# Optimization experiments

Hardware: AMD Instinct MI355X
Metric: run time of the kernel (lower is better)

## Reference

```python
import jax, jax.numpy as jnp
import numpy as np

N_HEAD = 16
N_KV_HEAD = 4
HEAD_DIM = 128
RMS_EPS = 1.1920928955078125e-07  # torch float32 eps used by F.rms_norm default


def apply_rotary_emb(x, cos, sin):
    # x: [B,T,H,D]; cos/sin: [1,T,1,D/2]
    d = x.shape[-1] // 2
    x1, x2 = x[..., :d], x[..., d:]
    return jnp.concatenate([x1 * cos + x2 * sin, -x1 * sin + x2 * cos], axis=-1)


def rms_norm(x):
    return x * jax.lax.rsqrt(jnp.mean(x * x, axis=-1, keepdims=True) + RMS_EPS)


def setup_inputs() -> dict:
    key = jax.random.key(0)
    ks = jax.random.split(key, 7)
    B, T, C = 2, 2048, 2048
    return {
        "x": jax.random.normal(ks[0], (B, T, C), jnp.float32),
        "cos": jax.random.normal(ks[1], (1, T, 1, HEAD_DIM // 2), jnp.float32),
        "sin": jax.random.normal(ks[2], (1, T, 1, HEAD_DIM // 2), jnp.float32),
        "wq": jax.random.normal(ks[3], (C, N_HEAD * HEAD_DIM), jnp.float32) * 0.02,
        "wk": jax.random.normal(ks[4], (C, N_KV_HEAD * HEAD_DIM), jnp.float32) * 0.02,
        "wv": jax.random.normal(ks[5], (C, N_KV_HEAD * HEAD_DIM), jnp.float32) * 0.02,
        "wo": jax.random.normal(ks[6], (C, C), jnp.float32) * 0.02,
        "window_size": 512,
    }


def reference(x, cos, sin, wq, wk, wv, wo, window_size):
    B, T, C = x.shape
    H, KV, D = N_HEAD, N_KV_HEAD, HEAD_DIM
    rep = H // KV
    q = (x @ wq).reshape(B, T, H, D)
    k = (x @ wk).reshape(B, T, KV, D)
    v = (x @ wv).reshape(B, T, KV, D)
    q = rms_norm(apply_rotary_emb(q, cos, sin))
    k = rms_norm(apply_rotary_emb(k, cos, sin))
    # GQA: group query heads by kv head instead of materializing expanded K/V
    qg = q.reshape(B, T, KV, rep, D)
    scale = 1.0 / np.sqrt(D)
    scores = jnp.einsum('btkrd,bskd->bkrts', qg, k) * scale  # [B,KV,rep,T,S]
    row = jnp.arange(T)[:, None]
    col = jnp.arange(T)[None, :]
    mask = (col <= row) & (row - col <= window_size)  # causal & sliding window
    scores = jnp.where(mask, scores, jnp.finfo(scores.dtype).min)
    probs = jax.nn.softmax(scores, axis=-1)
    y = jnp.einsum('bkrts,bskd->btkrd', probs, v).reshape(B, T, H * D)
    return y @ wo
```

## Files before the change

### kernel.cpp

```cpp
#include <hip/hip_runtime.h>
#include <stdint.h>

typedef __attribute__((ext_vector_type(4))) float f32x4;
typedef __attribute__((ext_vector_type(8))) __bf16 bf16x8;
typedef __attribute__((ext_vector_type(4))) unsigned int u32x4;
typedef unsigned short u16;

#define B_DIM 2
#define T_DIM 2048
#define C_DIM 2048
#define H_Q   16
#define H_KV  4
#define HD    128
#define NQKV  3072
#define MTOK  4096
#define RMS_EPS 1.1920928955078125e-07f

__device__ __forceinline__ u16 f2bf(float f) {
  union { float f; unsigned int u; } v; v.f = f;
  unsigned int r = v.u + 0x7FFFu + ((v.u >> 16) & 1u);
  return (u16)(r >> 16);
}
__device__ __forceinline__ float bf2f(u16 h) {
  union { unsigned int u; float f; } v; v.u = ((unsigned int)h) << 16;
  return v.f;
}
__device__ __forceinline__ f32x4 mfma16(bf16x8 a, bf16x8 b, f32x4 c) {
  return __builtin_amdgcn_mfma_f32_16x16x32_bf16(a, b, c, 0, 0, 0);
}

__global__ __launch_bounds__(256) void cast_x_kernel(const float* __restrict__ x,
                                                     u16* __restrict__ xb, int n) {
  int i = (blockIdx.x * 256 + threadIdx.x) * 4;
  if (i >= n) return;
  float4 v = *(const float4*)(x + i);
  u16 o0 = f2bf(v.x), o1 = f2bf(v.y), o2 = f2bf(v.z), o3 = f2bf(v.w);
  unsigned int lo = (unsigned int)o0 | ((unsigned int)o1 << 16);
  unsigned int hi = (unsigned int)o2 | ((unsigned int)o3 << 16);
  *(uint2*)(xb + i) = make_uint2(lo, hi);
}

__global__ __launch_bounds__(256) void transpose_cast_kernel(const float* __restrict__ in,
                                                             u16* __restrict__ out,
                                                             int K, int N) {
  __shared__ float tile[64][65];
  int n0 = blockIdx.x * 64, k0 = blockIdx.y * 64;
  int t = threadIdx.x;
  #pragma unroll
  for (int idx = t; idx < 4096; idx += 256) {
    int r = idx >> 6, c = idx & 63;
    tile[r][c] = in[(size_t)(k0 + r) * N + n0 + c];
  }
  __syncthreads();
  #pragma unroll
  for (int idx = t; idx < 4096; idx += 256) {
    int r = idx >> 6, c = idx & 63;
    out[(size_t)(n0 + r) * K + k0 + c] = f2bf(tile[c][r]);
  }
}

__global__ __launch_bounds__(256) void rope_rms_kernel(u16* __restrict__ qkv,
                                                       const float* __restrict__ cosb,
                                                       const float* __restrict__ sinb) {
  int gw = (blockIdx.x * 256 + threadIdx.x) >> 6;
  int lane = threadIdx.x & 63;
  int hh = gw % (H_Q + H_KV);
  int tok = gw / (H_Q + H_KV);
  int t = tok & (T_DIM - 1);
  int base = (hh < H_Q) ? hh * HD : (C_DIM + (hh - H_Q) * HD);
  u16* p = qkv + (size_t)tok * NQKV + base;
  float x1 = bf2f(p[lane]);
  float x2 = bf2f(p[lane + 64]);
  float c = cosb[t * 64 + lane];
  float s = sinb[t * 64 + lane];
  float o1 =  x1 * c + x2 * s;
  float o2 = -x1 * s + x2 * c;
  float ss = o1 * o1 + o2 * o2;
  #pragma unroll
  for (int off = 1; off < 64; off <<= 1) ss += __shfl_xor(ss, off);
  float r = rsqrtf(ss * (1.0f / 128.0f) + RMS_EPS);
  p[lane]      = f2bf(o1 * r);
  p[lane + 64] = f2bf(o2 * r);
}

template<int BF16OUT>
__global__ __launch_bounds__(256) void gemm_bt_kernel(const u16* __restrict__ A,
                                                      const u16* __restrict__ Bt,
                                                      void* __restrict__ Cv,
                                                      int M, int N, int K) {
  __shared__ __align__(16) u16 Asm[128 * 64];
  __shared__ __align__(16) u16 Bsm[128 * 64];
  const int tid = threadIdx.x;
  const int lane = tid & 63;
  const int wid = tid >> 6;
  const int m0 = blockIdx.y * 128, n0 = blockIdx.x * 128;
  const int wm = (wid >> 1) * 64, wn = (wid & 1) * 64;
  const int l15 = lane & 15, l4 = lane >> 4;
  f32x4 acc[4][4] = {};

  for (int k0 = 0; k0 < K; k0 += 64) {
    __syncthreads();
    #pragma unroll
    for (int i = 0; i < 4; ++i) {
      int cid = tid + i * 256;
      int row = cid >> 3, c = cid & 7;
      int dst = row * 128 + ((c ^ (row & 7)) * 16);
      u32x4 va = *(const u32x4*)(A  + (size_t)(m0 + row) * K + k0 + c * 8);
      *(u32x4*)((char*)Asm + dst) = va;
      u32x4 vb = *(const u32x4*)(Bt + (size_t)(n0 + row) * K + k0 + c * 8);
      *(u32x4*)((char*)Bsm + dst) = vb;
    }
    __syncthreads();
    #pragma unroll
    for (int ks = 0; ks < 2; ++ks) {
      bf16x8 af[4], bfr[4];
      #pragma unroll
      for (int mf = 0; mf < 4; ++mf) {
        int r = wm + mf * 16 + l15;
        int bo = r * 128 + (((ks * 4 + l4) ^ (r & 7)) * 16);
        af[mf] = __builtin_bit_cast(bf16x8, *(const u32x4*)((const char*)Asm + bo));
      }
      #pragma unroll
      for (int nf = 0; nf < 4; ++nf) {
        int r = wn + nf * 16 + l15;
        int bo = r * 128 + (((ks * 4 + l4) ^ (r & 7)) * 16);
        bfr[nf] = __builtin_bit_cast(bf16x8, *(const u32x4*)((const char*)Bsm + bo));
      }
      #pragma unroll
      for (int mf = 0; mf < 4; ++mf)
        #pragma unroll
        for (int nf = 0; nf < 4; ++nf)
          acc[mf][nf] = mfma16(af[mf], bfr[nf], acc[mf][nf]);
    }
  }
  #pragma unroll
  for (int mf = 0; mf < 4; ++mf)
    #pragma unroll
    for (int nf = 0; nf < 4; ++nf)
      #pragma unroll
      for (int reg = 0; reg < 4; ++reg) {
        int row = m0 + wm + mf * 16 + l4 * 4 + reg;
        int col = n0 + wn + nf * 16 + l15;
        float v = acc[mf][nf][reg];
        if (BF16OUT) ((u16*)Cv)[(size_t)row * N + col] = f2bf(v);
        else         ((float*)Cv)[(size_t)row * N + col] = v;
      }
}

__global__ __launch_bounds__(256) void attn_kernel(const u16* __restrict__ qkv,
                                                   u16* __restrict__ yb,
                                                   const int* __restrict__ wsz_p) {
  __shared__ __align__(16) u16 Ksm[64 * 128];
  __shared__ __align__(16) u16 Vsm[128 * 64];
  __shared__ __align__(16) u16 Psm[4 * 16 * 64];

  const int W = wsz_p[0];
  const int tid = threadIdx.x, lane = tid & 63, wid = tid >> 6;
  const int l15 = lane & 15, l4 = lane >> 4;
  const int bid = blockIdx.x;
  const int qt  = bid & 31;
  const int h   = (bid >> 5) & 15;
  const int b   = bid >> 9;
  const int kvh = h >> 2;
  const size_t tokb = (size_t)b * T_DIM;

  bf16x8 qf[4];
  {
    int r = qt * 64 + wid * 16 + l15;
    const u16* qp = qkv + (tokb + r) * NQKV + h * HD;
    #pragma unroll
    for (int ks = 0; ks < 4; ++ks)
      qf[ks] = __builtin_bit_cast(bf16x8, *(const u32x4*)(qp + ks * 32 + l4 * 8));
  }

  f32x4 yacc[8] = {};
  float mrow[4], lrow[4];
  #pragma unroll
  for (int rg = 0; rg < 4; ++rg) { mrow[rg] = -3.0e38f; lrow[rg] = 0.0f; }

  const float sc = 0.08838834764831845f * 1.4426950408889634f;
  const int rbase = qt * 64 + wid * 16;
  int smin = qt * 64 - W; if (smin < 0) smin = 0;
  const int t0 = smin >> 6;

  for (int kt = t0; kt <= qt; ++kt) {
    __syncthreads();
    {
      const u16* kp = qkv + (tokb + kt * 64) * NQKV + C_DIM + kvh * HD;
      #pragma unroll
      for (int i = 0; i < 4; ++i) {
        int cid = tid + i * 256;
        int key = cid >> 4, c = cid & 15;
        u32x4 v = *(const u32x4*)(kp + (size_t)key * NQKV + c * 8);
        *(u32x4*)((char*)Ksm + key * 256 + ((c ^ (key & 7)) * 16)) = v;
      }
    }
    {
      const u16* vp = qkv + (tokb + kt * 64) * NQKV + C_DIM + H_KV * HD + kvh * HD;
      int d = tid & 127, g = tid >> 7;
      #pragma unroll
      for (int cc = 0; cc < 4; ++cc) {
        int kc = g * 4 + cc;
        u16 vals[8];
        #pragma unroll
        for (int j = 0; j < 8; ++j)
          vals[j] = vp[(size_t)(kc * 8 + j) * NQKV + d];
        u32x4 w;
        w.x = (unsigned int)vals[0] | ((unsigned int)vals[1] << 16);
        w.y = (unsigned int)vals[2] | ((unsigned int)vals[3] << 16);
        w.z = (unsigned int)vals[4] | ((unsigned int)vals[5] << 16);
        w.w = (unsigned int)vals[6] | ((unsigned int)vals[7] << 16);
        *(u32x4*)((char*)Vsm + d * 128 + ((kc ^ (d & 7)) * 16)) = w;
      }
    }
    __syncthreads();

    float Sc[4][4];
    #pragma unroll
    for (int nf = 0; nf < 4; ++nf) {
      f32x4 sa = {0.f, 0.f, 0.f, 0.f};
      int key = nf * 16 + l15;
      #pragma unroll
      for (int ks = 0; ks < 4; ++ks) {
        int bo = key * 256 + (((ks * 4 + l4) ^ (key & 7)) * 16);
        bf16x8 kf = __builtin_bit_cast(bf16x8, *(const u32x4*)((const char*)Ksm + bo));
        sa = mfma16(qf[ks], kf, sa);
      }
      #pragma unroll
      for (int rg = 0; rg < 4; ++rg) Sc[nf][rg] = sa[rg] * sc;
    }

    const int slo = kt * 64;
    bool fullvalid = ((slo + 63) <= rbase) && ((rbase + 15 - slo) <= W);
    if (!fullvalid) {
      #pragma unroll
      for (int nf = 0; nf < 4; ++nf) {
        int s = slo + nf * 16 + l15;
        #pragma unroll
        for (int rg = 0; rg < 4; ++rg) {
          int r = rbase + l4 * 4 + rg;
          if (s > r || (r - s) > W) Sc[nf][rg] = -3.0e38f;
        }
      }
    }

    float f[4];
    #pragma unroll
    for (int rg = 0; rg < 4; ++rg) {
      float tm = fmaxf(fmaxf(Sc[0][rg], Sc[1][rg]), fmaxf(Sc[2][rg], Sc[3][rg]));
      #pragma unroll
      for (int off = 1; off < 16; off <<= 1) tm = fmaxf(tm, __shfl_xor(tm, off));
      float mnew = fmaxf(mrow[rg], tm);
      float mo = fmaxf(mrow[rg], -1.0e30f);
      float mc = fmaxf(mnew,     -1.0e30f);
      f[rg] = exp2f(mo - mc);
      mrow[rg] = mnew;
    }
    float rs[4] = {0.f, 0.f, 0.f, 0.f};
    u16 pb[4][4];
    #pragma unroll
    for (int nf = 0; nf < 4; ++nf)
      #pragma unroll
      for (int rg = 0; rg < 4; ++rg) {
        float mc = fmaxf(mrow[rg], -1.0e30f);
        float pv = exp2f(Sc[nf][rg] - mc);
        rs[rg] += pv;
        pb[nf][rg] = f2bf(pv);
      }
    #pragma unroll
    for (int rg = 0; rg < 4; ++rg) {
      #pragma unroll
      for (int off = 1; off < 16; off <<= 1) rs[rg] += __shfl_xor(rs[rg], off);
      lrow[rg] = lrow[rg] * f[rg] + rs[rg];
    }
    f32x4 fv = {f[0], f[1], f[2], f[3]};
    #pragma unroll
    for (int nf2 = 0; nf2 < 8; ++nf2) yacc[nf2] *= fv;

    char* pbase = (char*)Psm + wid * 2048;
    #pragma unroll
    for (int nf = 0; nf < 4; ++nf)
      #pragma unroll
      for (int rg = 0; rg < 4; ++rg) {
        int q   = l4 * 4 + rg;
        int key = nf * 16 + l15;
        int bo = q * 128 + ((((key >> 3) ^ (q & 7)) * 16) + (key & 7) * 2);
        *(u16*)(pbase + bo) = pb[nf][rg];
      }

    #pragma unroll
    for (int ks2 = 0; ks2 < 2; ++ks2) {
      int boA = l15 * 128 + (((ks2 * 4 + l4) ^ (l15 & 7)) * 16);
      bf16x8 pa = __builtin_bit_cast(bf16x8, *(const u32x4*)(pbase + boA));
      #pragma unroll
      for (int nf2 = 0; nf2 < 8; ++nf2) {
        int d = nf2 * 16 + l15;
        int boB = d * 128 + (((ks2 * 4 + l4) ^ (d & 7)) * 16);
        bf16x8 vf = __builtin_bit_cast(bf16x8, *(const u32x4*)((const char*)Vsm + boB));
        yacc[nf2] = mfma16(pa, vf, yacc[nf2]);
      }
    }
  }

  #pragma unroll
  for (int nf2 = 0; nf2 < 8; ++nf2)
    #pragma unroll
    for (int rg = 0; rg < 4; ++rg) {
      int r = qt * 64 + wid * 16 + l4 * 4 + rg;
      float v = yacc[nf2][rg] / lrow[rg];
      yb[(tokb + r) * (size_t)C_DIM + h * HD + nf2 * 16 + l15] = f2bf(v);
    }
}

extern "C" void kernel_launch(void* const* d_in, const int* in_sizes, int n_in,
                              void* d_out, int out_size, void* d_ws, size_t ws_size,
                              hipStream_t stream) {
  const float* x    = (const float*)d_in[0];
  const float* cosb = (const float*)d_in[1];
  const float* sinb = (const float*)d_in[2];
  const float* wq   = (const float*)d_in[3];
  const float* wk   = (const float*)d_in[4];
  const float* wv   = (const float*)d_in[5];
  const float* wo   = (const float*)d_in[6];
  const int*   wsz  = (const int*)d_in[7];

  char* ws = (char*)d_ws;
  u16* xb    = (u16*)(ws);
  u16* qkvb  = (u16*)(ws + (size_t)16777216);
  u16* wqkvb = (u16*)(ws + (size_t)41943040);
  u16* wob   = (u16*)(ws + (size_t)54525952);
  u16* ybuf  = (u16*)(ws + (size_t)62914560);

  cast_x_kernel<<<8192, 256, 0, stream>>>(x, xb, MTOK * C_DIM);
  transpose_cast_kernel<<<dim3(32, 32), 256, 0, stream>>>(wq, wqkvb, 2048, 2048);
  transpose_cast_kernel<<<dim3(8, 32), 256, 0, stream>>>(wk, wqkvb + (size_t)2048 * 2048, 2048, 512);
  transpose_cast_kernel<<<dim3(8, 32), 256, 0, stream>>>(wv, wqkvb + (size_t)2560 * 2048, 2048, 512);
  transpose_cast_kernel<<<dim3(32, 32), 256, 0, stream>>>(wo, wob, 2048, 2048);

  gemm_bt_kernel<1><<<dim3(NQKV / 128, MTOK / 128), 256, 0, stream>>>(xb, wqkvb, qkvb, MTOK, NQKV, C_DIM);
  rope_rms_kernel<<<(MTOK * (H_Q + H_KV)) / 4, 256, 0, stream>>>(qkvb, cosb, sinb);
  attn_kernel<<<B_DIM * H_Q * (T_DIM / 64), 256, 0, stream>>>(qkvb, ybuf, wsz);
  gemm_bt_kernel<0><<<dim3(C_DIM / 128, MTOK / 128), 256, 0, stream>>>(ybuf, wob, d_out, MTOK, C_DIM, C_DIM);
}
```

Before: 222.4 us.

## Use direct global-to-LDS loads, pre-transpose V, and double attention query tile

GEMM and attention tile loads now use global_load_lds to copy global memory straight into shared memory, with the XOR swizzle applied on the source column instead of the destination. A new kernel transposes V into a per-head [D,T] buffer (reusing the xb workspace) so attention can load V tiles with wide contiguous reads instead of strided 2-byte gathers. The attention block now covers 128 query rows, with each wave handling two 16-row fragments, so every K/V tile is reused twice as much. Key tiles that fall fully outside a wave's causal/window band are skipped. These changes add an extra launch, more registers per thread and fewer attention blocks in exchange.

```diff
diff --git a/kernel.cpp b/kernel.cpp
--- a/kernel.cpp
+++ b/kernel.cpp
@@ -27,6 +27,11 @@
 }
 __device__ __forceinline__ f32x4 mfma16(bf16x8 a, bf16x8 b, f32x4 c) {
   return __builtin_amdgcn_mfma_f32_16x16x32_bf16(a, b, c, 0, 0, 0);
+}
+__device__ __forceinline__ void gl_lds16(const void* g, void* l) {
+  __builtin_amdgcn_global_load_lds(
+      (const __attribute__((address_space(1))) unsigned int*)g,
+      (__attribute__((address_space(3))) unsigned int*)l, 16, 0, 0);
 }
 
 __global__ __launch_bounds__(256) void cast_x_kernel(const float* __restrict__ x,
@@ -83,6 +88,40 @@
   p[lane + 64] = f2bf(o2 * r);
 }
 
+__global__ __launch_bounds__(256) void vtrans_kernel(const u16* __restrict__ qkv,
+                                                     u16* __restrict__ vt) {
+  __shared__ __align__(16) u16 tile[64][136];
+  int bid = blockIdx.x;
+  int tt0 = (bid & 31) * 64;
+  int kvh = (bid >> 5) & 3;
+  int b   = bid >> 7;
+  const u16* vp = qkv + ((size_t)b * T_DIM + tt0) * NQKV + C_DIM + H_KV * HD + kvh * HD;
+  int tid = threadIdx.x;
+  #pragma unroll
+  for (int i = 0; i < 4; ++i) {
+    int cid = tid + i * 256;
+    int r = cid >> 4, c = cid & 15;
+    u32x4 v = *(const u32x4*)(vp + (size_t)r * NQKV + c * 8);
+    *(u32x4*)&tile[r][c * 8] = v;
+  }
+  __syncthreads();
+  u16* op = vt + ((size_t)(b * H_KV + kvh) * HD) * T_DIM + tt0;
+  #pragma unroll
+  for (int i = 0; i < 4; ++i) {
+    int cid = tid + i * 256;
+    int d = cid >> 3, tc = cid & 7;
+    u16 vals[8];
+    #pragma unroll
+    for (int j = 0; j < 8; ++j) vals[j] = tile[tc * 8 + j][d];
+    u32x4 w;
+    w.x = (unsigned int)vals[0] | ((unsigned int)vals[1] << 16);
+    w.y = (unsigned int)vals[2] | ((unsigned int)vals[3] << 16);
+    w.z = (unsigned int)vals[4] | ((unsigned int)vals[5] << 16);
+    w.w = (unsigned int)vals[6] | ((unsigned int)vals[7] << 16);
+    *(u32x4*)(op + (size_t)d * T_DIM + tc * 8) = w;
+  }
+}
+
 template<int BF16OUT>
 __global__ __launch_bounds__(256) void gemm_bt_kernel(const u16* __restrict__ A,
                                                       const u16* __restrict__ Bt,
@@ -96,19 +135,17 @@
   const int m0 = blockIdx.y * 128, n0 = blockIdx.x * 128;
   const int wm = (wid >> 1) * 64, wn = (wid & 1) * 64;
   const int l15 = lane & 15, l4 = lane >> 4;
+  const int csrc = (lane & 7) ^ (lane >> 3);
   f32x4 acc[4][4] = {};
 
   for (int k0 = 0; k0 < K; k0 += 64) {
     __syncthreads();
     #pragma unroll
     for (int i = 0; i < 4; ++i) {
-      int cid = tid + i * 256;
-      int row = cid >> 3, c = cid & 7;
-      int dst = row * 128 + ((c ^ (row & 7)) * 16);
-      u32x4 va = *(const u32x4*)(A  + (size_t)(m0 + row) * K + k0 + c * 8);
-      *(u32x4*)((char*)Asm + dst) = va;
-      u32x4 vb = *(const u32x4*)(Bt + (size_t)(n0 + row) * K + k0 + c * 8);
-      *(u32x4*)((char*)Bsm + dst) = vb;
+      int g = wid * 4 + i;
+      int row = g * 8 + (lane >> 3);
+      gl_lds16(A  + (size_t)(m0 + row) * K + k0 + csrc * 8, (char*)Asm + g * 1024);
+      gl_lds16(Bt + (size_t)(n0 + row) * K + k0 + csrc * 8, (char*)Bsm + g * 1024);
     }
     __syncthreads();
     #pragma unroll
@@ -148,168 +185,170 @@
 }
 
 __global__ __launch_bounds__(256) void attn_kernel(const u16* __restrict__ qkv,
+                                                   const u16* __restrict__ vt,
                                                    u16* __restrict__ yb,
                                                    const int* __restrict__ wsz_p) {
   __shared__ __align__(16) u16 Ksm[64 * 128];
   __shared__ __align__(16) u16 Vsm[128 * 64];
-  __shared__ __align__(16) u16 Psm[4 * 16 * 64];
+  __shared__ __align__(16) u16 Psm[4 * 32 * 64];
 
   const int W = wsz_p[0];
   const int tid = threadIdx.x, lane = tid & 63, wid = tid >> 6;
   const int l15 = lane & 15, l4 = lane >> 4;
   const int bid = blockIdx.x;
-  const int qt  = bid & 31;
-  const int h   = (bid >> 5) & 15;
-  const int b   = bid >> 9;
+  const int qt  = bid & 15;
+  const int h   = (bid >> 4) & 15;
+  const int b   = bid >> 8;
   const int kvh = h >> 2;
   const size_t tokb = (size_t)b * T_DIM;
-
-  bf16x8 qf[4];
-  {
-    int r = qt * 64 + wid * 16 + l15;
+  const u16* vtb = vt + ((size_t)(b * H_KV + kvh) * HD) * T_DIM;
+  const int rbase = qt * 128 + wid * 32;
+
+  bf16x8 qf[2][4];
+  #pragma unroll
+  for (int mf = 0; mf < 2; ++mf) {
+    int r = rbase + mf * 16 + l15;
     const u16* qp = qkv + (tokb + r) * NQKV + h * HD;
     #pragma unroll
     for (int ks = 0; ks < 4; ++ks)
-      qf[ks] = __builtin_bit_cast(bf16x8, *(const u32x4*)(qp + ks * 32 + l4 * 8));
-  }
-
-  f32x4 yacc[8] = {};
-  float mrow[4], lrow[4];
-  #pragma unroll
-  for (int rg = 0; rg < 4; ++rg) { mrow[rg] = -3.0e38f; lrow[rg] = 0.0f; }
+      qf[mf][ks] = __builtin_bit_cast(bf16x8, *(const u32x4*)(qp + ks * 32 + l4 * 8));
+  }
+
+  f32x4 yacc[2][8] = {};
+  float mrow[2][4], lrow[2][4];
+  #pragma unroll
+  for (int mf = 0; mf < 2; ++mf)
+    #pragma unroll
+    for (int rg = 0; rg < 4; ++rg) { mrow[mf][rg] = -3.0e38f; lrow[mf][rg] = 0.0f; }
 
   const float sc = 0.08838834764831845f * 1.4426950408889634f;
-  const int rbase = qt * 64 + wid * 16;
-  int smin = qt * 64 - W; if (smin < 0) smin = 0;
+  int smin = qt * 128 - W; if (smin < 0) smin = 0;
   const int t0 = smin >> 6;
-
-  for (int kt = t0; kt <= qt; ++kt) {
+  const int t1 = qt * 2 + 1;
+
+  for (int kt = t0; kt <= t1; ++kt) {
     __syncthreads();
     {
       const u16* kp = qkv + (tokb + kt * 64) * NQKV + C_DIM + kvh * HD;
       #pragma unroll
       for (int i = 0; i < 4; ++i) {
-        int cid = tid + i * 256;
-        int key = cid >> 4, c = cid & 15;
-        u32x4 v = *(const u32x4*)(kp + (size_t)key * NQKV + c * 8);
-        *(u32x4*)((char*)Ksm + key * 256 + ((c ^ (key & 7)) * 16)) = v;
+        int g = wid * 4 + i;
+        int row = g * 4 + (lane >> 4);
+        int cs = (lane & 15) ^ (row & 15);
+        gl_lds16(kp + (size_t)row * NQKV + cs * 8, (char*)Ksm + g * 1024);
       }
     }
     {
-      const u16* vp = qkv + (tokb + kt * 64) * NQKV + C_DIM + H_KV * HD + kvh * HD;
-      int d = tid & 127, g = tid >> 7;
-      #pragma unroll
-      for (int cc = 0; cc < 4; ++cc) {
-        int kc = g * 4 + cc;
-        u16 vals[8];
-        #pragma unroll
-        for (int j = 0; j < 8; ++j)
-          vals[j] = vp[(size_t)(kc * 8 + j) * NQKV + d];
-        u32x4 w;
-        w.x = (unsigned int)vals[0] | ((unsigned int)vals[1] << 16);
-        w.y = (unsigned int)vals[2] | ((unsigned int)vals[3] << 16);
-        w.z = (unsigned int)vals[4] | ((unsigned int)vals[5] << 16);
-        w.w = (unsigned int)vals[6] | ((unsigned int)vals[7] << 16);
-        *(u32x4*)((char*)Vsm + d * 128 + ((kc ^ (d & 7)) * 16)) = w;
+      const u16* vp = vtb + kt * 64;
+      #pragma unroll
+      for (int i = 0; i < 4; ++i) {
+        int g = wid * 4 + i;
+        int d = g * 8 + (lane >> 3);
+        int cs = (lane & 7) ^ (d & 7);
+        gl_lds16(vp + (size_t)d * T_DIM + cs * 8, (char*)Vsm + g * 1024);
       }
     }
     __syncthreads();
 
-    float Sc[4][4];
-    #pragma unroll
-    for (int nf = 0; nf < 4; ++nf) {
-      f32x4 sa = {0.f, 0.f, 0.f, 0.f};
-      int key = nf * 16 + l15;
-      #pragma unroll
-      for (int ks = 0; ks < 4; ++ks) {
-        int bo = key * 256 + (((ks * 4 + l4) ^ (key & 7)) * 16);
-        bf16x8 kf = __builtin_bit_cast(bf16x8, *(const u32x4*)((const char*)Ksm + bo));
-        sa = mfma16(qf[ks], kf, sa);
-      }
-      #pragma unroll
-      for (int rg = 0; rg < 4; ++rg) Sc[nf][rg] = sa[rg] * sc;
-    }
-
     const int slo = kt * 64;
-    bool fullvalid = ((slo + 63) <= rbase) && ((rbase + 15 - slo) <= W);
-    if (!fullvalid) {
-      #pragma unroll
-      for (int nf = 0; nf < 4; ++nf) {
-        int s = slo + nf * 16 + l15;
+    bool active = (slo <= rbase + 31) && ((rbase - (slo + 63)) <= W);
+    if (active) {
+      float fmul[2][4];
+      char* pbase = (char*)Psm + wid * 4096;
+      #pragma unroll
+      for (int mf = 0; mf < 2; ++mf) {
+        const int rb = rbase + mf * 16;
+        float Sc[4][4];
+        #pragma unroll
+        for (int nf = 0; nf < 4; ++nf) {
+          f32x4 sa = {0.f, 0.f, 0.f, 0.f};
+          int key = nf * 16 + l15;
+          #pragma unroll
+          for (int ks = 0; ks < 4; ++ks) {
+            int bo = key * 256 + (((ks * 4 + l4) ^ (key & 15)) * 16);
+            bf16x8 kf = __builtin_bit_cast(bf16x8, *(const u32x4*)((const char*)Ksm + bo));
+            sa = mfma16(qf[mf][ks], kf, sa);
+          }
+          #pragma unroll
+          for (int rg = 0; rg < 4; ++rg) Sc[nf][rg] = sa[rg] * sc;
+        }
+        bool fullvalid = ((slo + 63) <= rb) && ((rb + 15 - slo) <= W);
+        if (!fullvalid) {
+          #pragma unroll
+          for (int nf = 0; nf < 4; ++nf) {
+            int s = slo + nf * 16 + l15;
+            #pragma unroll
+            for (int rg = 0; rg < 4; ++rg) {
+              int r = rb + l4 * 4 + rg;
+              if (s > r || (r - s) > W) Sc[nf][rg] = -3.0e38f;
+            }
+          }
+        }
         #pragma unroll
         for (int rg = 0; rg < 4; ++rg) {
-          int r = rbase + l4 * 4 + rg;
-          if (s > r || (r - s) > W) Sc[nf][rg] = -3.0e38f;
-        }
-      }
-    }
-
-    float f[4];
-    #pragma unroll
-    for (int rg = 0; rg < 4; ++rg) {
-      float tm = fmaxf(fmaxf(Sc[0][rg], Sc[1][rg]), fmaxf(Sc[2][rg], Sc[3][rg]));
-      #pragma unroll
-      for (int off = 1; off < 16; off <<= 1) tm = fmaxf(tm, __shfl_xor(tm, off));
-      float mnew = fmaxf(mrow[rg], tm);
-      float mo = fmaxf(mrow[rg], -1.0e30f);
-      float mc = fmaxf(mnew,     -1.0e30f);
-      f[rg] = exp2f(mo - mc);
-      mrow[rg] = mnew;
-    }
-    float rs[4] = {0.f, 0.f, 0.f, 0.f};
-    u16 pb[4][4];
-    #pragma unroll
-    for (int nf = 0; nf < 4; ++nf)
+          float tm = fmaxf(fmaxf(Sc[0][rg], Sc[1][rg]), fmaxf(Sc[2][rg], Sc[3][rg]));
+          #pragma unroll
+          for (int off = 1; off < 16; off <<= 1) tm = fmaxf(tm, __shfl_xor(tm, off));
+          float mnew = fmaxf(mrow[mf][rg], tm);
+          float mo = fmaxf(mrow[mf][rg], -1.0e30f);
+          float mc = fmaxf(mnew,         -1.0e30f);
+          fmul[mf][rg] = exp2f(mo - mc);
+          mrow[mf][rg] = mnew;
+        }
+        float rs[4] = {0.f, 0.f, 0.f, 0.f};
+        #pragma unroll
+        for (int nf = 0; nf < 4; ++nf)
+          #pragma unroll
+          for (int rg = 0; rg < 4; ++rg) {
+            float mc = fmaxf(mrow[mf][rg], -1.0e30f);
+            float pv = exp2f(Sc[nf][rg] - mc);
+            rs[rg] += pv;
+            int q   = mf * 16 + l4 * 4 + rg;
+            int key = nf * 16 + l15;
+            int bo = q * 128 + (((key >> 3) ^ (q & 7)) * 16) + (key & 7) * 2;
+            *(u16*)(pbase + bo) = f2bf(pv);
+          }
+        #pragma unroll
+        for (int rg = 0; rg < 4; ++rg) {
+          #pragma unroll
+          for (int off = 1; off < 16; off <<= 1) rs[rg] += __shfl_xor(rs[rg], off);
+          lrow[mf][rg] = lrow[mf][rg] * fmul[mf][rg] + rs[rg];
+        }
+        f32x4 fv = {fmul[mf][0], fmul[mf][1], fmul[mf][2], fmul[mf][3]};
+        #pragma unroll
+        for (int nf2 = 0; nf2 < 8; ++nf2) yacc[mf][nf2] *= fv;
+      }
+      #pragma unroll
+      for (int ks2 = 0; ks2 < 2; ++ks2) {
+        bf16x8 pa[2];
+        #pragma unroll
+        for (int mf = 0; mf < 2; ++mf) {
+          int qr = mf * 16 + l15;
+          int boA = qr * 128 + (((ks2 * 4 + l4) ^ (qr & 7)) * 16);
+          pa[mf] = __builtin_bit_cast(bf16x8, *(const u32x4*)(pbase + boA));
+        }
+        #pragma unroll
+        for (int nf2 = 0; nf2 < 8; ++nf2) {
+          int d = nf2 * 16 + l15;
+          int boB = d * 128 + (((ks2 * 4 + l4) ^ (d & 7)) * 16);
+          bf16x8 vf = __builtin_bit_cast(bf16x8, *(const u32x4*)((const char*)Vsm + boB));
+          yacc[0][nf2] = mfma16(pa[0], vf, yacc[0][nf2]);
+          yacc[1][nf2] = mfma16(pa[1], vf, yacc[1][nf2]);
+        }
+      }
+    }
+  }
+
+  #pragma unroll
+  for (int mf = 0; mf < 2; ++mf)
+    #pragma unroll
+    for (int nf2 = 0; nf2 < 8; ++nf2)
       #pragma unroll
       for (int rg = 0; rg < 4; ++rg) {
-        float mc = fmaxf(mrow[rg], -1.0e30f);
-        float pv = exp2f(Sc[nf][rg] - mc);
-        rs[rg] += pv;
-        pb[nf][rg] = f2bf(pv);
-      }
-    #pragma unroll
-    for (int rg = 0; rg < 4; ++rg) {
-      #pragma unroll
-      for (int off = 1; off < 16; off <<= 1) rs[rg] += __shfl_xor(rs[rg], off);
-      lrow[rg] = lrow[rg] * f[rg] + rs[rg];
-    }
-    f32x4 fv = {f[0], f[1], f[2], f[3]};
-    #pragma unroll
-    for (int nf2 = 0; nf2 < 8; ++nf2) yacc[nf2] *= fv;
-
-    char* pbase = (char*)Psm + wid * 2048;
-    #pragma unroll
-    for (int nf = 0; nf < 4; ++nf)
-      #pragma unroll
-      for (int rg = 0; rg < 4; ++rg) {
-        int q   = l4 * 4 + rg;
-        int key = nf * 16 + l15;
-        int bo = q * 128 + ((((key >> 3) ^ (q & 7)) * 16) + (key & 7) * 2);
-        *(u16*)(pbase + bo) = pb[nf][rg];
-      }
-
-    #pragma unroll
-    for (int ks2 = 0; ks2 < 2; ++ks2) {
-      int boA = l15 * 128 + (((ks2 * 4 + l4) ^ (l15 & 7)) * 16);
-      bf16x8 pa = __builtin_bit_cast(bf16x8, *(const u32x4*)(pbase + boA));
-      #pragma unroll
-      for (int nf2 = 0; nf2 < 8; ++nf2) {
-        int d = nf2 * 16 + l15;
-        int boB = d * 128 + (((ks2 * 4 + l4) ^ (d & 7)) * 16);
-        bf16x8 vf = __builtin_bit_cast(bf16x8, *(const u32x4*)((const char*)Vsm + boB));
-        yacc[nf2] = mfma16(pa, vf, yacc[nf2]);
-      }
-    }
-  }
-
-  #pragma unroll
-  for (int nf2 = 0; nf2 < 8; ++nf2)
-    #pragma unroll
-    for (int rg = 0; rg < 4; ++rg) {
-      int r = qt * 64 + wid * 16 + l4 * 4 + rg;
-      float v = yacc[nf2][rg] / lrow[rg];
-      yb[(tokb + r) * (size_t)C_DIM + h * HD + nf2 * 16 + l15] = f2bf(v);
-    }
+        int r = rbase + mf * 16 + l4 * 4 + rg;
+        float v = yacc[mf][nf2][rg] / lrow[mf][rg];
+        yb[(tokb + r) * (size_t)C_DIM + h * HD + nf2 * 16 + l15] = f2bf(v);
+      }
 }
 
 extern "C" void kernel_launch(void* const* d_in, const int* in_sizes, int n_in,
@@ -330,6 +369,7 @@
   u16* wqkvb = (u16*)(ws + (size_t)41943040);
   u16* wob   = (u16*)(ws + (size_t)54525952);
   u16* ybuf  = (u16*)(ws + (size_t)62914560);
+  u16* vtb   = (u16*)(ws);
 
   cast_x_kernel<<<8192, 256, 0, stream>>>(x, xb, MTOK * C_DIM);
   transpose_cast_kernel<<<dim3(32, 32), 256, 0, stream>>>(wq, wqkvb, 2048, 2048);
@@ -339,6 +379,7 @@
 
   gemm_bt_kernel<1><<<dim3(NQKV / 128, MTOK / 128), 256, 0, stream>>>(xb, wqkvb, qkvb, MTOK, NQKV, C_DIM);
   rope_rms_kernel<<<(MTOK * (H_Q + H_KV)) / 4, 256, 0, stream>>>(qkvb, cosb, sinb);
-  attn_kernel<<<B_DIM * H_Q * (T_DIM / 64), 256, 0, stream>>>(qkvb, ybuf, wsz);
+  vtrans_kernel<<<B_DIM * H_KV * (T_DIM / 64), 256, 0, stream>>>(qkvb, vtb);
+  attn_kernel<<<B_DIM * H_Q * (T_DIM / 128), 256, 0, stream>>>(qkvb, vtb, ybuf, wsz);
   gemm_bt_kernel<0><<<dim3(C_DIM / 128, MTOK / 128), 256, 0, stream>>>(ybuf, wob, d_out, MTOK, C_DIM, C_DIM);
 }
```

Result: slower. 239.3 us (+7.6%).
